# Performance work log

Hardware: AMD Instinct MI355X
Metric: run time of the kernel (lower is better)

Reference implementation:

```python
import jax, jax.numpy as jnp
import numpy as np

N = 20000
E = 320000
DIN = 256
DH = 64
DOUT = 64
H = 8
NEG_SLOPE = 0.2


def _glorot(key, shape):
    fan_in, fan_out = shape[0], shape[-1]
    lim = jnp.sqrt(6.0 / (fan_in + fan_out))
    return jax.random.uniform(key, shape, jnp.float32, -lim, lim)


def setup_inputs() -> dict:
    key = jax.random.key(0)
    ks = jax.random.split(key, 12)
    x = jax.random.normal(ks[0], (N, DIN), jnp.float32)
    edge_index = jax.random.randint(ks[1], (2, E), 0, N, jnp.int32)
    # layer 1: dim_in -> heads*dim_h
    Wl1 = _glorot(ks[2], (DIN, H * DH));  bl1 = jnp.zeros((H * DH,), jnp.float32)
    Wr1 = _glorot(ks[3], (DIN, H * DH));  br1 = jnp.zeros((H * DH,), jnp.float32)
    att1 = _glorot(ks[4], (H, DH))
    bias1 = jnp.zeros((H * DH,), jnp.float32)
    # layer 2: heads*dim_h -> heads*dim_out
    Wl2 = _glorot(ks[5], (H * DH, H * DOUT)); bl2 = jnp.zeros((H * DOUT,), jnp.float32)
    Wr2 = _glorot(ks[6], (H * DH, H * DOUT)); br2 = jnp.zeros((H * DOUT,), jnp.float32)
    att2 = _glorot(ks[7], (H, DOUT))
    bias2 = jnp.zeros((H * DOUT,), jnp.float32)
    return dict(x=x, edge_index=edge_index, Wl1=Wl1, bl1=bl1, Wr1=Wr1, br1=br1,
                att1=att1, bias1=bias1, Wl2=Wl2, bl2=bl2, Wr2=Wr2, br2=br2,
                att2=att2, bias2=bias2)


def _gatv2(x, src, dst, Wl, bl, Wr, br, att, bias_out, heads, out_ch):
    n = x.shape[0]
    l = (x @ Wl + bl).reshape(n, heads, out_ch)   # source transform
    r = (x @ Wr + br).reshape(n, heads, out_ch)   # target transform
    # per-edge GATv2 score: att . LeakyReLU(l_j + r_i)
    e = jax.nn.leaky_relu(l[src] + r[dst], NEG_SLOPE)      # [E, H, C]
    logits = jnp.einsum('ehc,hc->eh', e, att)              # [E, H]
    # segmented softmax over incoming edges of each destination node
    m = jax.ops.segment_max(logits, dst, num_segments=n)   # [N, H]
    expd = jnp.exp(logits - m[dst])
    denom = jax.ops.segment_sum(expd, dst, num_segments=n)
    alpha = expd / denom[dst]                              # [E, H]
    msg = l[src] * alpha[:, :, None]                       # [E, H, C]
    out = jax.ops.segment_sum(msg, dst, num_segments=n)    # [N, H, C]
    return out.reshape(n, heads * out_ch) + bias_out


def reference(x, edge_index, Wl1, bl1, Wr1, br1, att1, bias1,
              Wl2, bl2, Wr2, br2, att2, bias2):
    n = x.shape[0]
    loops = jnp.arange(n, dtype=edge_index.dtype)
    src = jnp.concatenate([edge_index[0], loops])  # GATv2Conv adds self-loops
    dst = jnp.concatenate([edge_index[1], loops])
    # dropout is identity at inference
    h = _gatv2(x, src, dst, Wl1, bl1, Wr1, br1, att1, bias1, H, DH)
    h = jax.nn.elu(h)
    h = _gatv2(h, src, dst, Wl2, bl2, Wr2, br2, att2, bias2, H, DOUT)
    return h, jax.nn.log_softmax(h, axis=1)
```

## Files before the change

### kernel.cpp

```cpp
#include <hip/hip_runtime.h>
#include <math.h>

#define NN   20000
#define NE   320000
#define ET   (NE + NN)
#define D_IN 256
#define DHID 512
#define NLR  1024
#define MPAD 20096

typedef __attribute__((ext_vector_type(8))) short bf16x8;
typedef __attribute__((ext_vector_type(4))) float f32x4;

typedef __attribute__((address_space(3))) uint       lds_uint;
typedef __attribute__((address_space(1))) const uint gbl_uint;
#define ASYNC16(gp, lp) \
    __builtin_amdgcn_global_load_lds((gbl_uint*)(gp), (lds_uint*)(lp), 16, 0, 0)

__device__ __forceinline__ ushort f2bf(float f) {
    uint u = __float_as_uint(f);
    return (ushort)((u + 0x7fffu + ((u >> 16) & 1u)) >> 16);
}


__global__ __launch_bounds__(256) void init_count(int* count) {
    int i = blockIdx.x * 256 + threadIdx.x;
    if (i < NN) count[i] = 1;
}

__global__ __launch_bounds__(256) void hist_kernel(const int* __restrict__ dstv,
                                                   int* __restrict__ count) {
    int e = blockIdx.x * 256 + threadIdx.x;
    if (e < NE) atomicAdd(&count[dstv[e]], 1);
}

__global__ __launch_bounds__(1024) void scan_kernel(const int* __restrict__ count,
                                                    int* __restrict__ offs,
                                                    int* __restrict__ cursor) {
    __shared__ int sm[1024];
    const int CH = 20;
    int t = threadIdx.x;
    int base = t * CH;
    int local[CH];
    int s = 0;
#pragma unroll
    for (int i = 0; i < CH; i++) {
        int idx = base + i;
        int v = (idx < NN) ? count[idx] : 0;
        local[i] = s;
        s += v;
    }
    sm[t] = s;
    __syncthreads();
    for (int o = 1; o < 1024; o <<= 1) {
        int v = (t >= o) ? sm[t - o] : 0;
        __syncthreads();
        sm[t] += v;
        __syncthreads();
    }
    int pref = (t > 0) ? sm[t - 1] : 0;
#pragma unroll
    for (int i = 0; i < CH; i++) {
        int idx = base + i;
        if (idx < NN) {
            int o_ = pref + local[i];
            offs[idx] = o_;
            cursor[idx] = o_;
        }
    }
    if (t == 1023) offs[NN] = sm[1023];
}

__global__ __launch_bounds__(256) void scatter_kernel(const int* __restrict__ srcv,
                                                      const int* __restrict__ dstv,
                                                      int* __restrict__ cursor,
                                                      int* __restrict__ csr_src) {
    int e = blockIdx.x * 256 + threadIdx.x;
    if (e >= ET) return;
    int s, d;
    if (e < NE) { s = srcv[e]; d = dstv[e]; }
    else        { s = e - NE;  d = s; }
    int pos = atomicAdd(&cursor[d], 1);
    csr_src[pos] = s;
}


__global__ __launch_bounds__(256) void convert_x(const float* __restrict__ x,
                                                 ushort* __restrict__ a) {
    long e = ((long)blockIdx.x * 256 + threadIdx.x) * 4;
    if (e >= (long)MPAD * D_IN) return;
    int row = (int)(e >> 8);
    float4 v = make_float4(0.f, 0.f, 0.f, 0.f);
    if (row < NN) v = *(const float4*)&x[e];
    ushort4 o;
    o.x = f2bf(v.x); o.y = f2bf(v.y); o.z = f2bf(v.z); o.w = f2bf(v.w);
    *(ushort4*)&a[e] = o;
}

__global__ __launch_bounds__(256) void zero_pad2(ushort* __restrict__ a) {
    int t = blockIdx.x * 256 + threadIdx.x;
    if (t < (MPAD - NN) * DHID / 4) {
        ushort4 z = {0, 0, 0, 0};
        *(ushort4*)&a[(long)NN * DHID + (long)t * 4] = z;
    }
}

__global__ __launch_bounds__(256) void transpose_w(const float* __restrict__ Wl,
                                                   const float* __restrict__ Wr,
                                                   ushort* __restrict__ Wt, int K) {
    __shared__ float tile[32][33];
    int k0 = blockIdx.x * 32, n0 = blockIdx.y * 32;
    int tx = threadIdx.x & 31, ty = threadIdx.x >> 5;
    const float* __restrict__ W = (n0 < DHID) ? Wl : Wr;
    int nb = (n0 < DHID) ? n0 : n0 - DHID;
#pragma unroll
    for (int r = ty; r < 32; r += 8)
        tile[r][tx] = W[(long)(k0 + r) * DHID + nb + tx];
    __syncthreads();
#pragma unroll
    for (int r = ty; r < 32; r += 8)
        Wt[(long)(n0 + r) * K + k0 + tx] = f2bf(tile[tx][r]);
}


#define BM 128
#define BN 128
#define BK 64

__global__ __launch_bounds__(256) void gemm_mfma(const ushort* __restrict__ A, int K,
                                                 const ushort* __restrict__ Wt,
                                                 const float* __restrict__ bl,
                                                 const float* __restrict__ br,
                                                 ushort* __restrict__ out) {
    __shared__ ushort As[BM * BK];
    __shared__ ushort Bs[BN * BK];

    int t = threadIdx.x;
    int row0 = blockIdx.x * BM;
    int col0 = blockIdx.y * BN;

    int lane = t & 63, w = t >> 6;
    int wr = w >> 1, wc = w & 1;
    int l16 = lane & 15, lhi = lane >> 4;

    f32x4 acc[4][4];
#pragma unroll
    for (int m = 0; m < 4; m++)
#pragma unroll
        for (int n = 0; n < 4; n++)
            acc[m][n] = (f32x4){0.f, 0.f, 0.f, 0.f};

    for (int k0 = 0; k0 < K; k0 += BK) {
#pragma unroll
        for (int q = 0; q < 4; q++) {
            int chunk = q * 256 + t;
            int row = chunk >> 3;
            int il = (chunk & 7) ^ (row & 7);
            ASYNC16(A  + (long)(row0 + row) * K + k0 + il * 8, (char*)As + chunk * 16);
            ASYNC16(Wt + (long)(col0 + row) * K + k0 + il * 8, (char*)Bs + chunk * 16);
        }
        __syncthreads();
#pragma unroll
        for (int kk = 0; kk < 2; kk++) {
            bf16x8 af[4], bfr[4];
#pragma unroll
            for (int m = 0; m < 4; m++) {
                int rl = wr * 64 + m * 16 + l16;
                int off = rl * 128 + ((kk * 64 + lhi * 16) ^ ((rl & 7) << 4));
                af[m] = *(const bf16x8*)((const char*)As + off);
            }
#pragma unroll
            for (int n = 0; n < 4; n++) {
                int rl = wc * 64 + n * 16 + l16;
                int off = rl * 128 + ((kk * 64 + lhi * 16) ^ ((rl & 7) << 4));
                bfr[n] = *(const bf16x8*)((const char*)Bs + off);
            }
#pragma unroll
            for (int m = 0; m < 4; m++)
#pragma unroll
                for (int n = 0; n < 4; n++)
                    acc[m][n] = __builtin_amdgcn_mfma_f32_16x16x32_bf16(af[m], bfr[n], acc[m][n], 0, 0, 0);
        }
        __syncthreads();
    }

    float bvn[4];
#pragma unroll
    for (int n = 0; n < 4; n++) {
        int col = col0 + wc * 64 + n * 16 + l16;
        bvn[n] = (col < DHID) ? bl[col] : br[col - DHID];
    }
#pragma unroll
    for (int m = 0; m < 4; m++) {
        int rbase = row0 + wr * 64 + m * 16 + lhi * 4;
#pragma unroll
        for (int j = 0; j < 4; j++) {
            int row = rbase + j;
            if (row < NN) {
#pragma unroll
                for (int n = 0; n < 4; n++) {
                    int col = col0 + wc * 64 + n * 16 + l16;
                    out[(long)row * NLR + col] = f2bf(acc[m][n][j] + bvn[n]);
                }
            }
        }
    }
}


#define CVT8(u, f)                                  \
    f[0] = __uint_as_float((u).x << 16);            \
    f[1] = __uint_as_float((u).x & 0xffff0000u);    \
    f[2] = __uint_as_float((u).y << 16);            \
    f[3] = __uint_as_float((u).y & 0xffff0000u);    \
    f[4] = __uint_as_float((u).z << 16);            \
    f[5] = __uint_as_float((u).z & 0xffff0000u);    \
    f[6] = __uint_as_float((u).w << 16);            \
    f[7] = __uint_as_float((u).w & 0xffff0000u);

template <int MODE>
__global__ __launch_bounds__(256) void aggregate_kernel(const ushort* __restrict__ lr,
                                                        const float* __restrict__ att,
                                                        const float* __restrict__ bias,
                                                        const int* __restrict__ csr_src,
                                                        const int* __restrict__ offs,
                                                        ushort* __restrict__ out_bf,
                                                        float* __restrict__ out_f32) {
    int i = blockIdx.x * 4 + (threadIdx.x >> 6);
    int lane = threadIdx.x & 63;
    int c0 = lane << 3;

    uint4 ur = *(const uint4*)(lr + (long)i * NLR + DHID + c0);
    float rv[8];
    CVT8(ur, rv);
    float av[8];
    *(float4*)&av[0] = *(const float4*)&att[c0];
    *(float4*)&av[4] = *(const float4*)&att[c0 + 4];

    int beg = offs[i], end = offs[i + 1];
    float m = -3.0e38f, d = 0.f;
    float acc[8] = {0.f, 0.f, 0.f, 0.f, 0.f, 0.f, 0.f, 0.f};

    int j = csr_src[beg];
    uint4 v = *(const uint4*)(lr + (long)j * NLR + c0);

    for (int k = beg; k < end; k++) {
        uint4 vc = v;
        int kn = (k + 1 < end) ? k + 1 : k;
        int jn = csr_src[kn];
        v = *(const uint4*)(lr + (long)jn * NLR + c0);

        float lx[8];
        CVT8(vc, lx);
        float s = 0.f;
#pragma unroll
        for (int c = 0; c < 8; c++) {
            float e = lx[c] + rv[c];
            e = fmaxf(e, 0.2f * e);
            s = fmaf(av[c], e, s);
        }
        s *= 1.44269504f;
        s += __shfl_xor(s, 1);
        s += __shfl_xor(s, 2);
        s += __shfl_xor(s, 4);

        if (s > m) {
            float sc = exp2f(m - s);
            d *= sc;
#pragma unroll
            for (int c = 0; c < 8; c++) acc[c] *= sc;
            m = s;
        }
        float wgt = exp2f(s - m);
        d += wgt;
#pragma unroll
        for (int c = 0; c < 8; c++) acc[c] = fmaf(wgt, lx[c], acc[c]);
    }

    float inv = 1.f / d;
    float o[8];
#pragma unroll
    for (int c = 0; c < 8; c++) o[c] = fmaf(acc[c], inv, bias[c0 + c]);

    if (MODE == 0) {
#pragma unroll
        for (int c = 0; c < 8; c++) o[c] = (o[c] > 0.f) ? o[c] : expm1f(o[c]);
        uint4 p;
        p.x = (uint)f2bf(o[0]) | ((uint)f2bf(o[1]) << 16);
        p.y = (uint)f2bf(o[2]) | ((uint)f2bf(o[3]) << 16);
        p.z = (uint)f2bf(o[4]) | ((uint)f2bf(o[5]) << 16);
        p.w = (uint)f2bf(o[6]) | ((uint)f2bf(o[7]) << 16);
        *(uint4*)(out_bf + (long)i * DHID + c0) = p;
    } else {
        *(float4*)&out_f32[(long)i * DHID + c0] = *(float4*)&o[0];
        *(float4*)&out_f32[(long)i * DHID + c0 + 4] = *(float4*)&o[4];
    }
}


__global__ __launch_bounds__(64) void logsoftmax_kernel(const float* __restrict__ h,
                                                        float* __restrict__ out) {
    int i = blockIdx.x;
    int t = threadIdx.x;
    float v[8];
    float m = -3.0e38f;
#pragma unroll
    for (int k = 0; k < 8; k++) {
        v[k] = h[(long)i * DHID + t + 64 * k];
        m = fmaxf(m, v[k]);
    }
#pragma unroll
    for (int o = 32; o; o >>= 1) m = fmaxf(m, __shfl_xor(m, o));
    float s = 0.f;
#pragma unroll
    for (int k = 0; k < 8; k++) s += __expf(v[k] - m);
#pragma unroll
    for (int o = 32; o; o >>= 1) s += __shfl_xor(s, o);
    float lg = logf(s);
#pragma unroll
    for (int k = 0; k < 8; k++) out[(long)i * DHID + t + 64 * k] = v[k] - m - lg;
}


extern "C" void kernel_launch(void* const* d_in, const int* in_sizes, int n_in,
                              void* d_out, int out_size, void* d_ws, size_t ws_size,
                              hipStream_t stream) {
    const float* x     = (const float*)d_in[0];
    const int*   ei    = (const int*)d_in[1];
    const float* Wl1   = (const float*)d_in[2];
    const float* bl1   = (const float*)d_in[3];
    const float* Wr1   = (const float*)d_in[4];
    const float* br1   = (const float*)d_in[5];
    const float* att1  = (const float*)d_in[6];
    const float* bias1 = (const float*)d_in[7];
    const float* Wl2   = (const float*)d_in[8];
    const float* bl2   = (const float*)d_in[9];
    const float* Wr2   = (const float*)d_in[10];
    const float* br2   = (const float*)d_in[11];
    const float* att2  = (const float*)d_in[12];
    const float* bias2 = (const float*)d_in[13];

    float* out = (float*)d_out;
    float* h2  = out;
    float* lsm = out + (long)NN * DHID;

    ushort* lrbuf  = (ushort*)d_ws;
    ushort* Abf    = lrbuf + (long)NN * NLR;
    ushort* Wt1    = Abf + (long)MPAD * DHID;
    ushort* Wt2    = Wt1 + (long)NLR * D_IN;
    int*    csr_src = (int*)(Wt2 + (long)NLR * DHID);
    int*    count   = csr_src + ET;
    int*    offs    = count + NN;
    int*    cursor  = offs + NN + 1;

    const int* srcv = ei;
    const int* dstv = ei + NE;

    convert_x<<<(MPAD * D_IN / 4 + 255) / 256, 256, 0, stream>>>(x, Abf);
    zero_pad2<<<((MPAD - NN) * DHID / 4 + 255) / 256, 256, 0, stream>>>(Abf);
    transpose_w<<<dim3(D_IN / 32, NLR / 32), 256, 0, stream>>>(Wl1, Wr1, Wt1, D_IN);
    transpose_w<<<dim3(DHID / 32, NLR / 32), 256, 0, stream>>>(Wl2, Wr2, Wt2, DHID);

    init_count<<<(NN + 255) / 256, 256, 0, stream>>>(count);
    hist_kernel<<<(NE + 255) / 256, 256, 0, stream>>>(dstv, count);
    scan_kernel<<<1, 1024, 0, stream>>>(count, offs, cursor);
    scatter_kernel<<<(ET + 255) / 256, 256, 0, stream>>>(srcv, dstv, cursor, csr_src);

    dim3 ggrid((NN + BM - 1) / BM, NLR / BN);

    gemm_mfma<<<ggrid, 256, 0, stream>>>(Abf, D_IN, Wt1, bl1, br1, lrbuf);
    aggregate_kernel<0><<<NN / 4, 256, 0, stream>>>(lrbuf, att1, bias1, csr_src, offs, Abf, nullptr);

    gemm_mfma<<<ggrid, 256, 0, stream>>>(Abf, DHID, Wt2, bl2, br2, lrbuf);
    aggregate_kernel<1><<<NN / 4, 256, 0, stream>>>(lrbuf, att2, bias2, csr_src, offs, nullptr, h2);

    logsoftmax_kernel<<<NN, 64, 0, stream>>>(h2, lsm);
}
```

Measured before the change: 270.0 us.

## Fuse log-softmax into layer-2 aggregation and simplify edge softmax math

The row log-softmax now runs inside the second aggregation kernel, so the separate logsoftmax launch and its reread of h2 are gone. The LeakyReLU score is rewritten as 0.6*t + 0.4*|t|, with the log2(e) factor folded into precomputed attention vectors. The online softmax only rescales when the running max grows by more than 8, which drops most rescale branches at the cost of allowing weights up to 2^8. The prefetch index clamp is removed, so csr_src[end] is read one past the last edge of the final node, and the bias load is vectorised.

Result: faster. 262.8 us (-2.7%).

```diff
diff --git a/kernel.cpp b/kernel.cpp
--- a/kernel.cpp
+++ b/kernel.cpp
@@ -225,7 +225,8 @@
                                                         const int* __restrict__ csr_src,
                                                         const int* __restrict__ offs,
                                                         ushort* __restrict__ out_bf,
-                                                        float* __restrict__ out_f32) {
+                                                        float* __restrict__ out_f32,
+                                                        float* __restrict__ out_lsm) {
     int i = blockIdx.x * 4 + (threadIdx.x >> 6);
     int lane = threadIdx.x & 63;
     int c0 = lane << 3;
@@ -233,9 +234,14 @@
     uint4 ur = *(const uint4*)(lr + (long)i * NLR + DHID + c0);
     float rv[8];
     CVT8(ur, rv);
-    float av[8];
-    *(float4*)&av[0] = *(const float4*)&att[c0];
-    *(float4*)&av[4] = *(const float4*)&att[c0 + 4];
+    float a06[8], a04[8];
+    float4 at0 = *(const float4*)&att[c0];
+    float4 at1 = *(const float4*)&att[c0 + 4];
+    const float K06 = 0.6f * 1.44269504f, K04 = 0.4f * 1.44269504f;
+    a06[0] = at0.x * K06; a06[1] = at0.y * K06; a06[2] = at0.z * K06; a06[3] = at0.w * K06;
+    a06[4] = at1.x * K06; a06[5] = at1.y * K06; a06[6] = at1.z * K06; a06[7] = at1.w * K06;
+    a04[0] = at0.x * K04; a04[1] = at0.y * K04; a04[2] = at0.z * K04; a04[3] = at0.w * K04;
+    a04[4] = at1.x * K04; a04[5] = at1.y * K04; a04[6] = at1.z * K04; a04[7] = at1.w * K04;
 
     int beg = offs[i], end = offs[i + 1];
     float m = -3.0e38f, d = 0.f;
@@ -246,8 +252,7 @@
 
     for (int k = beg; k < end; k++) {
         uint4 vc = v;
-        int kn = (k + 1 < end) ? k + 1 : k;
-        int jn = csr_src[kn];
+        int jn = csr_src[k + 1];
         v = *(const uint4*)(lr + (long)jn * NLR + c0);
 
         float lx[8];
@@ -255,23 +260,24 @@
         float s = 0.f;
 #pragma unroll
         for (int c = 0; c < 8; c++) {
-            float e = lx[c] + rv[c];
-            e = fmaxf(e, 0.2f * e);
-            s = fmaf(av[c], e, s);
-        }
-        s *= 1.44269504f;
+            float tt = lx[c] + rv[c];
+            s = fmaf(a06[c], tt, s);
+            s = fmaf(a04[c], __builtin_fabsf(tt), s);
+        }
         s += __shfl_xor(s, 1);
         s += __shfl_xor(s, 2);
         s += __shfl_xor(s, 4);
 
-        if (s > m) {
-            float sc = exp2f(m - s);
+        float delta = s - m;
+        if (__builtin_expect(delta > 8.f, 0)) {
+            float sc = exp2f(-delta);
             d *= sc;
 #pragma unroll
             for (int c = 0; c < 8; c++) acc[c] *= sc;
             m = s;
-        }
-        float wgt = exp2f(s - m);
+            delta = 0.f;
+        }
+        float wgt = exp2f(delta);
         d += wgt;
 #pragma unroll
         for (int c = 0; c < 8; c++) acc[c] = fmaf(wgt, lx[c], acc[c]);
@@ -279,8 +285,12 @@
 
     float inv = 1.f / d;
     float o[8];
-#pragma unroll
-    for (int c = 0; c < 8; c++) o[c] = fmaf(acc[c], inv, bias[c0 + c]);
+    float4 bi0 = *(const float4*)&bias[c0];
+    float4 bi1 = *(const float4*)&bias[c0 + 4];
+    o[0] = fmaf(acc[0], inv, bi0.x); o[1] = fmaf(acc[1], inv, bi0.y);
+    o[2] = fmaf(acc[2], inv, bi0.z); o[3] = fmaf(acc[3], inv, bi0.w);
+    o[4] = fmaf(acc[4], inv, bi1.x); o[5] = fmaf(acc[5], inv, bi1.y);
+    o[6] = fmaf(acc[6], inv, bi1.z); o[7] = fmaf(acc[7], inv, bi1.w);
 
     if (MODE == 0) {
 #pragma unroll
@@ -292,33 +302,25 @@
         p.w = (uint)f2bf(o[6]) | ((uint)f2bf(o[7]) << 16);
         *(uint4*)(out_bf + (long)i * DHID + c0) = p;
     } else {
-        *(float4*)&out_f32[(long)i * DHID + c0] = *(float4*)&o[0];
+        *(float4*)&out_f32[(long)i * DHID + c0]     = *(float4*)&o[0];
         *(float4*)&out_f32[(long)i * DHID + c0 + 4] = *(float4*)&o[4];
-    }
-}
-
-
-__global__ __launch_bounds__(64) void logsoftmax_kernel(const float* __restrict__ h,
-                                                        float* __restrict__ out) {
-    int i = blockIdx.x;
-    int t = threadIdx.x;
-    float v[8];
-    float m = -3.0e38f;
-#pragma unroll
-    for (int k = 0; k < 8; k++) {
-        v[k] = h[(long)i * DHID + t + 64 * k];
-        m = fmaxf(m, v[k]);
-    }
-#pragma unroll
-    for (int o = 32; o; o >>= 1) m = fmaxf(m, __shfl_xor(m, o));
-    float s = 0.f;
-#pragma unroll
-    for (int k = 0; k < 8; k++) s += __expf(v[k] - m);
-#pragma unroll
-    for (int o = 32; o; o >>= 1) s += __shfl_xor(s, o);
-    float lg = logf(s);
-#pragma unroll
-    for (int k = 0; k < 8; k++) out[(long)i * DHID + t + 64 * k] = v[k] - m - lg;
+        float mx = o[0];
+#pragma unroll
+        for (int c = 1; c < 8; c++) mx = fmaxf(mx, o[c]);
+#pragma unroll
+        for (int off = 1; off < 64; off <<= 1) mx = fmaxf(mx, __shfl_xor(mx, off));
+        float se = 0.f;
+#pragma unroll
+        for (int c = 0; c < 8; c++) se += __expf(o[c] - mx);
+#pragma unroll
+        for (int off = 1; off < 64; off <<= 1) se += __shfl_xor(se, off);
+        float lg = mx + logf(se);
+        float l0[8];
+#pragma unroll
+        for (int c = 0; c < 8; c++) l0[c] = o[c] - lg;
+        *(float4*)&out_lsm[(long)i * DHID + c0]     = *(float4*)&l0[0];
+        *(float4*)&out_lsm[(long)i * DHID + c0 + 4] = *(float4*)&l0[4];
+    }
 }
 
 
@@ -369,10 +371,8 @@
     dim3 ggrid((NN + BM - 1) / BM, NLR / BN);
 
     gemm_mfma<<<ggrid, 256, 0, stream>>>(Abf, D_IN, Wt1, bl1, br1, lrbuf);
-    aggregate_kernel<0><<<NN / 4, 256, 0, stream>>>(lrbuf, att1, bias1, csr_src, offs, Abf, nullptr);
+    aggregate_kernel<0><<<NN / 4, 256, 0, stream>>>(lrbuf, att1, bias1, csr_src, offs, Abf, nullptr, nullptr);
 
     gemm_mfma<<<ggrid, 256, 0, stream>>>(Abf, DHID, Wt2, bl2, br2, lrbuf);
-    aggregate_kernel<1><<<NN / 4, 256, 0, stream>>>(lrbuf, att2, bias2, csr_src, offs, nullptr, h2);
-
-    logsoftmax_kernel<<<NN, 64, 0, stream>>>(h2, lsm);
-}
+    aggregate_kernel<1><<<NN / 4, 256, 0, stream>>>(lrbuf, att2, bias2, csr_src, offs, nullptr, h2, lsm);
+}
```
